# Kernel optimization log

Measured on AMD Instinct MI355X. Metric: run time of the kernel, lower is better.

## Reference

```python
import jax, jax.numpy as jnp
import numpy as np

N_E = 1024
E_DIM = 256
BETA = 0.25

def setup_inputs() -> dict:
    key = jax.random.key(0)
    k1, k2 = jax.random.split(key)
    z = jax.random.normal(k1, (32, E_DIM, 32, 32), dtype=jnp.float32)
    # embedding initialized uniform(-1/n_e, 1/n_e) as in the torch module
    emb_w = jax.random.uniform(k2, (N_E, E_DIM), dtype=jnp.float32,
                               minval=-1.0 / N_E, maxval=1.0 / N_E)
    return {"z": z, "emb_w": emb_w}

def reference(z, emb_w):
    # z: (B, C, H, W) with C == e_dim
    zp = jnp.transpose(z, (0, 2, 3, 1))          # (B, H, W, C)
    zf = zp.reshape(-1, emb_w.shape[1])           # (N, e_dim)
    # squared L2 distances: ||z||^2 + ||e||^2 - 2 z e^T  -> (N, n_e)
    d = (jnp.sum(zf * zf, axis=1, keepdims=True)
         + jnp.sum(emb_w * emb_w, axis=1)
         - 2.0 * jnp.matmul(zf, emb_w.T))
    idx = jnp.argmin(d, axis=1)                   # (N,)
    min_encoding_indices = idx[:, None]           # (N, 1)
    min_encodings = jax.nn.one_hot(idx, emb_w.shape[0], dtype=zf.dtype)  # (N, n_e)
    z_q = emb_w[idx].reshape(zp.shape)            # gather instead of one-hot matmul
    # VQ loss (stop-gradient on codebook / encoder respectively)
    loss = (jnp.mean((jax.lax.stop_gradient(z_q) - zp) ** 2)
            + BETA * jnp.mean((z_q - jax.lax.stop_gradient(zp)) ** 2))
    # straight-through estimator
    z_q_st = zp + jax.lax.stop_gradient(z_q - zp)
    e_mean = jnp.mean(min_encodings, axis=0)      # (n_e,)
    perplexity = jnp.exp(-jnp.sum(e_mean * jnp.log(e_mean + 1e-10)))
    z_q_out = jnp.transpose(z_q_st, (0, 3, 1, 2)) # (B, C, H, W)
    return (z_q_out, loss, perplexity, min_encodings, min_encoding_indices)
```

## Files before the change

kernel.cpp:

```cpp
#include <hip/hip_runtime.h>
#include <math.h>

#define NROWS 32768
#define NE    1024
#define CDIM  256
#define ZB_STRIDE 262144

#define ZQ_OFF   0
#define LOSS_OFF 8388608
#define PERP_OFF 8388609
#define ENC_OFF  8388610
#define IDX_OFF  41943042

#define THETA 1.0e-4f
#define NEG2_SCALE (-0.00048828125f)

typedef _Float16 f16x8 __attribute__((ext_vector_type(8)));
typedef __attribute__((ext_vector_type(4))) float f32x4;
typedef __attribute__((ext_vector_type(8))) unsigned short ushort8;

__device__ __forceinline__ unsigned short f2h(float x) {
  _Float16 h = (_Float16)x;
  unsigned short u;
  __builtin_memcpy(&u, &h, 2);
  return u;
}

__device__ __forceinline__ float np_sumsq_256_s1(const float* __restrict__ base) {
  float tot[2];
#pragma unroll
  for (int hh = 0; hh < 2; ++hh) {
    float r[8];
#pragma unroll
    for (int j = 0; j < 8; ++j) {
      float x = base[hh * 128 + j];
      r[j] = __fmul_rn(x, x);
    }
    for (int i = 8; i < 128; i += 8) {
#pragma unroll
      for (int j = 0; j < 8; ++j) {
        float x = base[hh * 128 + i + j];
        r[j] = __fadd_rn(r[j], __fmul_rn(x, x));
      }
    }
    tot[hh] = __fadd_rn(__fadd_rn(__fadd_rn(r[0], r[1]), __fadd_rn(r[2], r[3])),
                        __fadd_rn(__fadd_rn(r[4], r[5]), __fadd_rn(r[6], r[7])));
  }
  return __fadd_rn(tot[0], tot[1]);
}

__global__ __launch_bounds__(256) void prep_e(const float* __restrict__ emb,
                                              unsigned short* __restrict__ ef16r,
                                              float* __restrict__ embT,
                                              float* __restrict__ enorm) {
  const int bid = blockIdx.x;
  const int t = threadIdx.x;
  if (bid < 128) {
    int cid = bid * 256 + t;
    int e = cid >> 5, cc = cid & 31;
    int kc = cc >> 2, g = cc & 3;
    int c0 = kc * 32 + g * 8;
    ushort8 o;
#pragma unroll
    for (int el = 0; el < 8; ++el) o[el] = f2h(emb[(size_t)e * 256 + c0 + el] * 4096.0f);
    int et = e >> 7, wcb = (e >> 6) & 1, nj = (e >> 4) & 3, l15e = e & 15;
    size_t chunk = ((((size_t)et * 2 + wcb) * 8 + kc) * 4 + nj) * 64 + (size_t)g * 16 + l15e;
    *reinterpret_cast<ushort8*>(ef16r + (chunk << 3)) = o;
  } else if (bid < 384) {
    __shared__ float tile[32][33];
    int tb = bid - 128;
    int be = tb & 31, bc = tb >> 5;
    int tx = t & 31, ty = t >> 5;
#pragma unroll
    for (int i = 0; i < 4; ++i)
      tile[ty + 8 * i][tx] = emb[(size_t)(be * 32 + ty + 8 * i) * 256 + bc * 32 + tx];
    __syncthreads();
#pragma unroll
    for (int i = 0; i < 4; ++i)
      embT[(size_t)(bc * 32 + ty + 8 * i) * 1024 + be * 32 + tx] = tile[tx][ty + 8 * i];
  } else {
    int n = (bid - 384) * 256 + t;
    enorm[n] = np_sumsq_256_s1(emb + (size_t)n * CDIM);
  }
}

__global__ __launch_bounds__(512, 4) void zconv_argmin(
    const float* __restrict__ z, const unsigned short* __restrict__ ef16r,
    const float* __restrict__ enorm, float* __restrict__ znorm,
    int* __restrict__ idx_out, float* __restrict__ loss_blk,
    int* __restrict__ flag_cnt, int* __restrict__ flag_list) {
  __shared__ __align__(16) char smA[34048];
  __shared__ float accsF[2][8][16][4];
  __shared__ float znl[64];
  __shared__ float sdd[64][8];
  __shared__ float sd2[64][8];
  __shared__ int   sdi[64][8];

  const int t = threadIdx.x;
  const int bid = blockIdx.x;
  const int mb = (bid & 7) * 64 + (bid >> 3);
  const int n0 = mb * 64;
  const int b = mb >> 4, hwt = mb & 15;
  const int hw0 = hwt * 64;

  unsigned short (*T16)[266] = reinterpret_cast<unsigned short (*)[266]>(smA);
  unsigned short* Bfrag = reinterpret_cast<unsigned short*>(smA);

  if (t < 256) {
    const int hw4 = t & 15;
    const int jj = (t >> 4) & 7;
    const int hh = t >> 7;
    const float* zb = z + (size_t)b * ZB_STRIDE + hw0 + hw4 * 4;
    float rr[4];
#pragma unroll
    for (int i = 0; i < 16; ++i) {
      int c = hh * 128 + jj + 8 * i;
      float4 v = *reinterpret_cast<const float4*>(zb + (size_t)c * 1024);
      const float xv[4] = {v.x, v.y, v.z, v.w};
#pragma unroll
      for (int q = 0; q < 4; ++q) {
        float p = __fmul_rn(xv[q], xv[q]);
        rr[q] = (i == 0) ? p : __fadd_rn(rr[q], p);
        T16[hw4 * 4 + q][c] = f2h(xv[q]);
      }
    }
#pragma unroll
    for (int q = 0; q < 4; ++q) accsF[hh][jj][hw4][q] = rr[q];
  }
  __syncthreads();

  if (t < 64) {
    const int h4 = t >> 2, cq = t & 3;
    float tot[2];
#pragma unroll
    for (int half = 0; half < 2; ++half) {
      float r[8];
#pragma unroll
      for (int j = 0; j < 8; ++j) r[j] = accsF[half][j][h4][cq];
      tot[half] = __fadd_rn(__fadd_rn(__fadd_rn(r[0], r[1]), __fadd_rn(r[2], r[3])),
                            __fadd_rn(__fadd_rn(r[4], r[5]), __fadd_rn(r[6], r[7])));
    }
    float nr = __fadd_rn(tot[0], tot[1]);
    znl[t] = nr;
    znorm[n0 + t] = nr;
  }
  ushort8 fr[8];
  {
    const int l15w = t & 15, gw = (t >> 4) & 3, miw = (t >> 6) & 3;
    const int rowW = miw * 16 + l15w;
    if (t < 256) {
#pragma unroll
      for (int kc = 0; kc < 8; ++kc)
#pragma unroll
        for (int el = 0; el < 8; ++el) fr[kc][el] = T16[rowW][kc * 32 + gw * 8 + el];
    }
  }
  __syncthreads();

  if (t < 256) {
    const int l15w = t & 15, gw = (t >> 4) & 3, miw = (t >> 6) & 3;
#pragma unroll
    for (int kc = 0; kc < 8; ++kc) {
      int chunk = (kc * 4 + miw) * 64 + gw * 16 + l15w;
      *reinterpret_cast<ushort8*>(Bfrag + chunk * 8) = fr[kc];
    }
  }
  __syncthreads();

  const int lane = t & 63, w = t >> 6;
  const int l15 = lane & 15, g = lane >> 4;

  float zn[4];
#pragma unroll
  for (int nj = 0; nj < 4; ++nj) zn[nj] = znl[nj * 16 + l15];

  float bd[4], b2[4]; int bi[4];
#pragma unroll
  for (int nj = 0; nj < 4; ++nj) { bd[nj] = 3.4e38f; b2[nj] = 3.4e38f; bi[nj] = 0; }

  const f32x4 z4 = {0.f, 0.f, 0.f, 0.f};
#pragma unroll 1
  for (int et = 0; et < 2; ++et) {
    const unsigned short* aP = ef16r + (size_t)(w * 2 + et) * 16384 + lane * 8;

    f32x4 acc[4][4];
#pragma unroll
    for (int ei = 0; ei < 4; ++ei)
#pragma unroll
      for (int nj = 0; nj < 4; ++nj) acc[ei][nj] = z4;

#pragma unroll 1
    for (int kc = 0; kc < 8; ++kc) {
      f16x8 af[4], bv[4];
#pragma unroll
      for (int ei = 0; ei < 4; ++ei)
        af[ei] = *reinterpret_cast<const f16x8*>(aP + ei * 512);
#pragma unroll
      for (int nj = 0; nj < 4; ++nj)
        bv[nj] = *reinterpret_cast<const f16x8*>(Bfrag + ((kc * 4 + nj) * 64 + lane) * 8);
      aP += 2048;
#pragma unroll
      for (int ei = 0; ei < 4; ++ei)
#pragma unroll
        for (int nj = 0; nj < 4; ++nj)
          acc[ei][nj] = __builtin_amdgcn_mfma_f32_16x16x32_f16(af[ei], bv[nj],
                                                               acc[ei][nj], 0, 0, 0);
    }

    const int e0w = (w * 2 + et) * 64;
#pragma unroll
    for (int ei = 0; ei < 4; ++ei)
#pragma unroll
      for (int rg = 0; rg < 4; ++rg) {
        int e = e0w + ei * 16 + g * 4 + rg;
        float en = enorm[e];
#pragma unroll
        for (int nj = 0; nj < 4; ++nj) {
          float d = fmaf(NEG2_SCALE, acc[ei][nj][rg], __fadd_rn(zn[nj], en));
          if (d < bd[nj]) {
            b2[nj] = bd[nj]; bd[nj] = d; bi[nj] = e;
          } else if (d < b2[nj]) {
            b2[nj] = d;
          }
        }
      }
  }

#pragma unroll
  for (int nj = 0; nj < 4; ++nj) {
#pragma unroll
    for (int m = 16; m <= 32; m <<= 1) {
      float od = __shfl_xor(bd[nj], m, 64);
      int   oi = __shfl_xor(bi[nj], m, 64);
      float o2 = __shfl_xor(b2[nj], m, 64);
      float hi = fmaxf(bd[nj], od);
      b2[nj] = fminf(fminf(b2[nj], o2), hi);
      if (od < bd[nj] || (od == bd[nj] && oi < bi[nj])) { bd[nj] = od; bi[nj] = oi; }
    }
    if (g == 0) {
      int nl = nj * 16 + l15;
      sdd[nl][w] = bd[nj];
      sdi[nl][w] = bi[nj];
      sd2[nl][w] = b2[nj];
    }
  }
  __syncthreads();

  if (t < 64) {
    float bdf = 3.4e38f; int bif = 0x7FFFFFFF; int bw = -1;
#pragma unroll
    for (int ww = 0; ww < 8; ++ww) {
      float d = sdd[t][ww];
      int   i = sdi[t][ww];
      if (d < bdf || (d == bdf && i < bif)) { bdf = d; bif = i; bw = ww; }
    }
    float b2f = 3.4e38f;
#pragma unroll
    for (int ww = 0; ww < 8; ++ww) {
      float v = (ww == bw) ? sd2[t][ww] : sdd[t][ww];
      b2f = fminf(b2f, v);
    }
    int n = n0 + t;
    idx_out[n] = bif;
    if (b2f - bdf < THETA) {
      int p = atomicAdd(flag_cnt, 1);
      flag_list[p] = n;
    }
    float s = bdf;
#pragma unroll
    for (int m = 1; m <= 32; m <<= 1) s += __shfl_xor(s, m, 64);
    if (t == 0) loss_blk[bid] = s;
  }
}

__global__ __launch_bounds__(256) void repair_kernel(
    const float* __restrict__ z, const float* __restrict__ embT,
    const float* __restrict__ znorm, const float* __restrict__ enorm,
    const int* __restrict__ flag_cnt, const int* __restrict__ flag_list,
    int* __restrict__ idx_out) {
  __shared__ float zrow[4][256];
  __shared__ float rd[256];
  __shared__ int   ri[256];
  const int t = threadIdx.x;
  const int cnt = flag_cnt[0] < NROWS ? flag_cnt[0] : NROWS;
  const int nquad = (cnt + 3) >> 2;
  const float4* embT4 = reinterpret_cast<const float4*>(embT);
  for (int j = blockIdx.x; j < nquad; j += gridDim.x) {
    int nr[4];
    __syncthreads();
#pragma unroll
    for (int r = 0; r < 4; ++r) {
      int jr = j * 4 + r;
      nr[r] = flag_list[jr < cnt ? jr : cnt - 1];
      zrow[r][t] = z[(size_t)(nr[r] >> 10) * ZB_STRIDE + (size_t)t * 1024 + (nr[r] & 1023)];
    }
    __syncthreads();
    float4 dot[4] = {{0.f,0.f,0.f,0.f},{0.f,0.f,0.f,0.f},{0.f,0.f,0.f,0.f},{0.f,0.f,0.f,0.f}};
    for (int k = 0; k < 256; ++k) {
      float4 v = embT4[k * 256 + t];
#pragma unroll
      for (int r = 0; r < 4; ++r) {
        float s = zrow[r][k];
        dot[r].x = fmaf(s, v.x, dot[r].x);
        dot[r].y = fmaf(s, v.y, dot[r].y);
        dot[r].z = fmaf(s, v.z, dot[r].z);
        dot[r].w = fmaf(s, v.w, dot[r].w);
      }
    }
#pragma unroll 1
    for (int r = 0; r < 4; ++r) {
      const float zn = znorm[nr[r]];
      float bd = 3.4e38f; int bi = 0;
      const float dv[4] = {dot[r].x, dot[r].y, dot[r].z, dot[r].w};
#pragma unroll
      for (int q = 0; q < 4; ++q) {
        int e = t * 4 + q;
        float d = __fsub_rn(__fadd_rn(zn, enorm[e]), __fmul_rn(2.0f, dv[q]));
        if (d < bd) { bd = d; bi = e; }
      }
      rd[t] = bd; ri[t] = bi;
      __syncthreads();
      for (int s2 = 128; s2 > 0; s2 >>= 1) {
        if (t < s2) {
          float od = rd[t + s2]; int oi = ri[t + s2];
          if (od < rd[t] || (od == rd[t] && oi < ri[t])) { rd[t] = od; ri[t] = oi; }
        }
        __syncthreads();
      }
      if (t == 0) idx_out[nr[r]] = ri[0];
      __syncthreads();
    }
  }
}

__global__ __launch_bounds__(256) void outputs_kernel(const int* __restrict__ idx,
                                                      const float* __restrict__ emb,
                                                      float* __restrict__ out_enc,
                                                      float* __restrict__ out_idxf,
                                                      int* __restrict__ hist,
                                                      float* __restrict__ zq_out) {
  const int t = threadIdx.x;
  for (int i = blockIdx.x * 256 + t; i < NROWS * 256; i += 2048 * 256) {
    int n = i >> 8, j4 = i & 255;
    int e = idx[n];
    float4 v = {0.f, 0.f, 0.f, 0.f};
    if ((e >> 2) == j4) ((float*)&v)[e & 3] = 1.0f;
    reinterpret_cast<float4*>(out_enc)[i] = v;
  }
  if (blockIdx.x < 1024) {
    __shared__ int   sidx[32];
    __shared__ float erow[32][257];
    int b = blockIdx.x >> 5, h = blockIdx.x & 31;
    if (t < 32) sidx[t] = idx[b * 1024 + h * 32 + t];
    __syncthreads();
    const float4* emb4 = reinterpret_cast<const float4*>(emb);
    int rj = t >> 3, v0 = t & 7;
    int er = sidx[rj];
#pragma unroll
    for (int u = 0; u < 8; ++u) {
      int f4 = v0 + 8 * u;
      float4 vv = emb4[(size_t)er * 64 + f4];
      erow[rj][f4 * 4 + 0] = vv.x;
      erow[rj][f4 * 4 + 1] = vv.y;
      erow[rj][f4 * 4 + 2] = vv.z;
      erow[rj][f4 * 4 + 3] = vv.w;
    }
    __syncthreads();
    int w4 = t & 7, cs = t >> 3;
    float4* zq4 = reinterpret_cast<float4*>(zq_out + (size_t)b * ZB_STRIDE + h * 32);
#pragma unroll
    for (int u = 0; u < 8; ++u) {
      int c = cs + 32 * u;
      float4 o = {erow[w4 * 4 + 0][c], erow[w4 * 4 + 1][c],
                  erow[w4 * 4 + 2][c], erow[w4 * 4 + 3][c]};
      zq4[(size_t)c * 256 + w4] = o;
    }
  } else if (blockIdx.x < 1152) {
    int n = (blockIdx.x - 1024) * 256 + t;
    int e = idx[n];
    out_idxf[n] = (float)e;
    atomicAdd(&hist[e], 1);
  }
}

__global__ __launch_bounds__(256) void finalize_kernel(const float* __restrict__ loss_blk,
                                                       const int* __restrict__ hist,
                                                       float* __restrict__ out_loss,
                                                       float* __restrict__ out_perp) {
  __shared__ float red[256];
  int t = threadIdx.x;
  red[t] = loss_blk[t] + loss_blk[t + 256];
  __syncthreads();
  for (int s2 = 128; s2 > 0; s2 >>= 1) {
    if (t < s2) red[t] += red[t + s2];
    __syncthreads();
  }
  if (t == 0) out_loss[0] = 1.25f * (red[0] / 8388608.0f);
  __syncthreads();
  float hs = 0.f;
  for (int i = t; i < 1024; i += 256) {
    float em = (float)hist[i] / 32768.0f;
    hs += em * logf(em + 1e-10f);
  }
  red[t] = hs;
  __syncthreads();
  for (int s2 = 128; s2 > 0; s2 >>= 1) {
    if (t < s2) red[t] += red[t + s2];
    __syncthreads();
  }
  if (t == 0) out_perp[0] = expf(-red[0]);
}

extern "C" void kernel_launch(void* const* d_in, const int* in_sizes, int n_in,
                              void* d_out, int out_size, void* d_ws, size_t ws_size,
                              hipStream_t stream) {
  const float* z   = (const float*)d_in[0];
  const float* emb = (const float*)d_in[1];
  float* out = (float*)d_out;

  float* out_zq   = out + ZQ_OFF;
  float* out_loss = out + LOSS_OFF;
  float* out_perp = out + PERP_OFF;
  float* out_enc  = out + ENC_OFF;
  float* out_idxf = out + IDX_OFF;

  int*   idx       = (int*)d_ws;
  int*   hist      = idx + NROWS;
  int*   flag_cnt  = hist + NE;
  int*   flag_list = flag_cnt + 4;
  float* loss_blk  = (float*)(flag_list + NROWS);
  float* znorm     = loss_blk + 512;
  float* enorm     = znorm + NROWS;

  unsigned short* ef16r = (unsigned short*)(out_enc + 2);
  float*          embT  = (float*)(ef16r + (size_t)NE * CDIM);

  hipMemsetAsync(hist, 0, (NE + 1) * sizeof(int), stream);

  prep_e<<<388, 256, 0, stream>>>(emb, ef16r, embT, enorm);
  zconv_argmin<<<512, 512, 0, stream>>>(z, ef16r, enorm, znorm,
                                        idx, loss_blk, flag_cnt, flag_list);
  repair_kernel<<<256, 256, 0, stream>>>(z, embT, znorm, enorm, flag_cnt, flag_list, idx);
  outputs_kernel<<<2048, 256, 0, stream>>>(idx, emb, out_enc, out_idxf, hist, out_zq);
  finalize_kernel<<<1, 256, 0, stream>>>(loss_blk, hist, out_loss, out_perp);
}
```

Before: 134.8 us.

## Fuse one-hot encoding, index and histogram writes into argmin kernel epilogue

The argmin kernel now writes the 128MB one-hot encodings, float indices and histogram counts directly in its epilogue, and the repair kernel patches only the rows whose index changed (zeroing the old one-hot entry and fixing the histogram). The separate outputs kernel is reduced to the z_q gather. This avoids re-reading the indices and lets the large one-hot store overlap with other blocks' compute. The fp16 codebook scratch is moved into the z_q output region so the early one-hot writes do not overwrite it. It adds serial store work to the tail of the argmin blocks.

Result: no change. 134.5 us (-0.3%).

```diff
diff --git a/kernel.cpp b/kernel.cpp
--- a/kernel.cpp
+++ b/kernel.cpp
@@ -88,13 +88,16 @@
     const float* __restrict__ z, const unsigned short* __restrict__ ef16r,
     const float* __restrict__ enorm, float* __restrict__ znorm,
     int* __restrict__ idx_out, float* __restrict__ loss_blk,
-    int* __restrict__ flag_cnt, int* __restrict__ flag_list) {
+    int* __restrict__ flag_cnt, int* __restrict__ flag_list,
+    float* __restrict__ out_enc, float* __restrict__ out_idxf,
+    int* __restrict__ hist) {
   __shared__ __align__(16) char smA[34048];
   __shared__ float accsF[2][8][16][4];
   __shared__ float znl[64];
   __shared__ float sdd[64][8];
   __shared__ float sd2[64][8];
   __shared__ int   sdi[64][8];
+  __shared__ int   sidx[64];
 
   const int t = threadIdx.x;
   const int bid = blockIdx.x;
@@ -262,6 +265,9 @@
     }
     int n = n0 + t;
     idx_out[n] = bif;
+    sidx[t] = bif;
+    out_idxf[n] = (float)bif;
+    atomicAdd(&hist[bif], 1);
     if (b2f - bdf < THETA) {
       int p = atomicAdd(flag_cnt, 1);
       flag_list[p] = n;
@@ -270,6 +276,17 @@
 #pragma unroll
     for (int m = 1; m <= 32; m <<= 1) s += __shfl_xor(s, m, 64);
     if (t == 0) loss_blk[bid] = s;
+  }
+  __syncthreads();
+
+  float4* enc4 = reinterpret_cast<float4*>(out_enc + (size_t)n0 * 1024);
+#pragma unroll 4
+  for (int i = t; i < 16384; i += 512) {
+    int nl = i >> 8, j4 = i & 255;
+    int e = sidx[nl];
+    float4 v = {0.f, 0.f, 0.f, 0.f};
+    if ((e >> 2) == j4) ((float*)&v)[e & 3] = 1.0f;
+    enc4[i] = v;
   }
 }
 
@@ -277,7 +294,8 @@
     const float* __restrict__ z, const float* __restrict__ embT,
     const float* __restrict__ znorm, const float* __restrict__ enorm,
     const int* __restrict__ flag_cnt, const int* __restrict__ flag_list,
-    int* __restrict__ idx_out) {
+    int* __restrict__ idx_out, float* __restrict__ out_enc,
+    float* __restrict__ out_idxf, int* __restrict__ hist) {
   __shared__ float zrow[4][256];
   __shared__ float rd[256];
   __shared__ int   ri[256];
@@ -327,59 +345,54 @@
         }
         __syncthreads();
       }
-      if (t == 0) idx_out[nr[r]] = ri[0];
+      if (t == 0 && (j * 4 + r) < cnt) {
+        int n = nr[r];
+        int oldv = idx_out[n];
+        int newv = ri[0];
+        if (newv != oldv) {
+          idx_out[n] = newv;
+          out_idxf[n] = (float)newv;
+          out_enc[(size_t)n * NE + oldv] = 0.f;
+          out_enc[(size_t)n * NE + newv] = 1.f;
+          atomicAdd(&hist[oldv], -1);
+          atomicAdd(&hist[newv], 1);
+        }
+      }
       __syncthreads();
     }
   }
 }
 
-__global__ __launch_bounds__(256) void outputs_kernel(const int* __restrict__ idx,
-                                                      const float* __restrict__ emb,
-                                                      float* __restrict__ out_enc,
-                                                      float* __restrict__ out_idxf,
-                                                      int* __restrict__ hist,
-                                                      float* __restrict__ zq_out) {
+__global__ __launch_bounds__(256) void zq_gather(const int* __restrict__ idx,
+                                                 const float* __restrict__ emb,
+                                                 float* __restrict__ zq_out) {
   const int t = threadIdx.x;
-  for (int i = blockIdx.x * 256 + t; i < NROWS * 256; i += 2048 * 256) {
-    int n = i >> 8, j4 = i & 255;
-    int e = idx[n];
-    float4 v = {0.f, 0.f, 0.f, 0.f};
-    if ((e >> 2) == j4) ((float*)&v)[e & 3] = 1.0f;
-    reinterpret_cast<float4*>(out_enc)[i] = v;
-  }
-  if (blockIdx.x < 1024) {
-    __shared__ int   sidx[32];
-    __shared__ float erow[32][257];
-    int b = blockIdx.x >> 5, h = blockIdx.x & 31;
-    if (t < 32) sidx[t] = idx[b * 1024 + h * 32 + t];
-    __syncthreads();
-    const float4* emb4 = reinterpret_cast<const float4*>(emb);
-    int rj = t >> 3, v0 = t & 7;
-    int er = sidx[rj];
-#pragma unroll
-    for (int u = 0; u < 8; ++u) {
-      int f4 = v0 + 8 * u;
-      float4 vv = emb4[(size_t)er * 64 + f4];
-      erow[rj][f4 * 4 + 0] = vv.x;
-      erow[rj][f4 * 4 + 1] = vv.y;
-      erow[rj][f4 * 4 + 2] = vv.z;
-      erow[rj][f4 * 4 + 3] = vv.w;
-    }
-    __syncthreads();
-    int w4 = t & 7, cs = t >> 3;
-    float4* zq4 = reinterpret_cast<float4*>(zq_out + (size_t)b * ZB_STRIDE + h * 32);
-#pragma unroll
-    for (int u = 0; u < 8; ++u) {
-      int c = cs + 32 * u;
-      float4 o = {erow[w4 * 4 + 0][c], erow[w4 * 4 + 1][c],
-                  erow[w4 * 4 + 2][c], erow[w4 * 4 + 3][c]};
-      zq4[(size_t)c * 256 + w4] = o;
-    }
-  } else if (blockIdx.x < 1152) {
-    int n = (blockIdx.x - 1024) * 256 + t;
-    int e = idx[n];
-    out_idxf[n] = (float)e;
-    atomicAdd(&hist[e], 1);
+  __shared__ int   sidx[32];
+  __shared__ float erow[32][257];
+  int b = blockIdx.x >> 5, h = blockIdx.x & 31;
+  if (t < 32) sidx[t] = idx[b * 1024 + h * 32 + t];
+  __syncthreads();
+  const float4* emb4 = reinterpret_cast<const float4*>(emb);
+  int rj = t >> 3, v0 = t & 7;
+  int er = sidx[rj];
+#pragma unroll
+  for (int u = 0; u < 8; ++u) {
+    int f4 = v0 + 8 * u;
+    float4 vv = emb4[(size_t)er * 64 + f4];
+    erow[rj][f4 * 4 + 0] = vv.x;
+    erow[rj][f4 * 4 + 1] = vv.y;
+    erow[rj][f4 * 4 + 2] = vv.z;
+    erow[rj][f4 * 4 + 3] = vv.w;
+  }
+  __syncthreads();
+  int w4 = t & 7, cs = t >> 3;
+  float4* zq4 = reinterpret_cast<float4*>(zq_out + (size_t)b * ZB_STRIDE + h * 32);
+#pragma unroll
+  for (int u = 0; u < 8; ++u) {
+    int c = cs + 32 * u;
+    float4 o = {erow[w4 * 4 + 0][c], erow[w4 * 4 + 1][c],
+                erow[w4 * 4 + 2][c], erow[w4 * 4 + 3][c]};
+    zq4[(size_t)c * 256 + w4] = o;
   }
 }
 
@@ -432,15 +445,17 @@
   float* znorm     = loss_blk + 512;
   float* enorm     = znorm + NROWS;
 
-  unsigned short* ef16r = (unsigned short*)(out_enc + 2);
+  unsigned short* ef16r = (unsigned short*)(out_zq + 2);
   float*          embT  = (float*)(ef16r + (size_t)NE * CDIM);
 
   hipMemsetAsync(hist, 0, (NE + 1) * sizeof(int), stream);
 
   prep_e<<<388, 256, 0, stream>>>(emb, ef16r, embT, enorm);
   zconv_argmin<<<512, 512, 0, stream>>>(z, ef16r, enorm, znorm,
-                                        idx, loss_blk, flag_cnt, flag_list);
-  repair_kernel<<<256, 256, 0, stream>>>(z, embT, znorm, enorm, flag_cnt, flag_list, idx);
-  outputs_kernel<<<2048, 256, 0, stream>>>(idx, emb, out_enc, out_idxf, hist, out_zq);
+                                        idx, loss_blk, flag_cnt, flag_list,
+                                        out_enc, out_idxf, hist);
+  repair_kernel<<<256, 256, 0, stream>>>(z, embT, znorm, enorm, flag_cnt, flag_list,
+                                         idx, out_enc, out_idxf, hist);
+  zq_gather<<<1024, 256, 0, stream>>>(idx, emb, out_zq);
   finalize_kernel<<<1, 256, 0, stream>>>(loss_blk, hist, out_loss, out_perp);
 }
```
